# Performance work log

Measured on AMD Instinct MI355X. Metric: run time of the kernel, lower is better.

Reference implementation:

```python
import jax, jax.numpy as jnp
import numpy as np
from jax import lax

# Orthonormal 2x2 Haar (db1). Analysis uses dwt_scale per coefficient; the
# synthesis uses 0.5*idwt_scale so that dwt_scale=0.5, idwt_scale=1.0 gives a
# perfect round trip (Hadamard matrix M, M@M = 4I, M symmetric).
DWT_SCALE = 0.5
IDWT_SCALE = 1.0
WT_LEVELS = 3
STRIDE = 1
PAD = 1  # (kernel_size - 1) // 2


def dwt2(x, s):
    # x: (B, C, H, W) -> (B, C, 4, H/2, W/2), subband order LL, LH, HL, HH
    a = x[..., 0::2, 0::2]
    b = x[..., 0::2, 1::2]
    c = x[..., 1::2, 0::2]
    d = x[..., 1::2, 1::2]
    ll = (a + b + c + d) * s
    lh = (a - b + c - d) * s
    hl = (a + b - c - d) * s
    hh = (a - b - c + d) * s
    return jnp.stack([ll, lh, hl, hh], axis=2)


def idwt2(sub, s):
    # sub: (B, C, 4, h, w) -> (B, C, 2h, 2w); inverse of dwt2 when s = 0.5/ (4*dwt_s) * ... here Hadamard symmetric
    ll, lh, hl, hh = sub[:, :, 0], sub[:, :, 1], sub[:, :, 2], sub[:, :, 3]
    a = (ll + lh + hl + hh) * s
    b = (ll - lh + hl - hh) * s
    c = (ll + lh - hl - hh) * s
    d = (ll - lh - hl + hh) * s
    B, C, h, w = a.shape
    row0 = jnp.stack([a, b], axis=-1).reshape(B, C, h, 2 * w)
    row1 = jnp.stack([c, d], axis=-1).reshape(B, C, h, 2 * w)
    return jnp.stack([row0, row1], axis=-2).reshape(B, C, 2 * h, 2 * w)


def conv2d(x, w, stride, pad):
    return lax.conv_general_dilated(
        x, w, window_strides=(stride, stride),
        padding=[(pad, pad), (pad, pad)],
        dimension_numbers=('NCHW', 'OIHW', 'NCHW'))


def wtconv_core(x, weight):
    cout4 = weight.shape[0]
    cout = cout4 // 4
    curr_ll = x
    ll_levels, high_levels = [], []
    for _ in range(WT_LEVELS):
        sub = dwt2(curr_ll, DWT_SCALE)             # (B, C, 4, h, w)
        B, C, _, h, w = sub.shape
        y = conv2d(sub.reshape(B, C * 4, h, w), weight, STRIDE, PAD)
        y = y.reshape(B, cout, 4, h, w)
        ll_levels.append(y[:, :, 0])
        high_levels.append(y[:, :, 1:])
        curr_ll = sub[:, :, 0]                     # pre-conv LL feeds next level
    next_ll = jnp.zeros_like(ll_levels[-1])
    for ll, hi in zip(reversed(ll_levels), reversed(high_levels)):
        ll = ll + next_ll
        sub = jnp.concatenate([ll[:, :, None], hi], axis=2)
        next_ll = idwt2(sub, 0.5 * IDWT_SCALE)
    return next_ll


def setup_inputs() -> dict:
    key = jax.random.key(0)
    k1, k2, k3 = jax.random.split(key, 3)
    B, C, H, W = 8, 32, 224, 224
    K = 3
    x = jax.random.normal(k1, (B, C, H, W), dtype=jnp.float32)
    fan_in = C * 4 * K * K
    bound = np.sqrt(6.0 / ((1.0 + 2.236 ** 2) * fan_in))
    weight = jax.random.uniform(k2, (C * 4, C * 4, K, K), dtype=jnp.float32,
                                minval=-bound, maxval=bound)
    bias = jax.random.normal(k3, (C,), dtype=jnp.float32) * 0.01
    return {"x": x, "weight": weight, "bias": bias}


def reference(x, weight, bias):
    H, W = x.shape[-2:]
    pad_factor = 2 ** WT_LEVELS
    pad_h = (pad_factor - H % pad_factor) % pad_factor
    pad_w = (pad_factor - W % pad_factor) % pad_factor
    xp = x
    if pad_h > 0 or pad_w > 0:
        xp = jnp.pad(x, ((0, 0), (0, 0), (0, pad_h), (0, pad_w)), mode='reflect')
    out = wtconv_core(xp, weight)
    out = out[..., :H, :W]
    return out + bias[None, :, None, None]
```

## Files before the change

kernel.cpp:

```cpp
#include <hip/hip_runtime.h>

typedef __bf16 bf16_t;
typedef __bf16 bf16x4_t __attribute__((ext_vector_type(4)));
typedef __bf16 bf16x8_t __attribute__((ext_vector_type(8)));
typedef float f32x16_t __attribute__((ext_vector_type(16)));

#define AS_G(p) ((const __attribute__((address_space(1))) void*)(p))
#define AS_L(p) ((__attribute__((address_space(3))) void*)(p))
#define DRAIN_VM() asm volatile("s_waitcnt vmcnt(0)" ::: "memory")

__device__ __forceinline__ void repack_body(const float* __restrict__ w,
                                            bf16_t* __restrict__ wt2,
                                            int o) {
  int e = o & 7;
  int lane = (o >> 3) & 63;
  int f = o >> 9;
  int wc = f & 1;
  int nt = (f >> 1) & 1;
  int kc = (f >> 2) & 3;
  int hk = (f >> 4) & 1;
  int t = f >> 5;
  int oc = wc * 64 + nt * 32 + (lane & 31);
  int ic = (hk * 8 + kc * 2 + (lane >> 5)) * 8 + e;
  wt2[o] = (bf16_t)w[((size_t)oc * 128 + ic) * 9 + t];
}

__device__ __forceinline__ void dwt_body(const float* __restrict__ in,
                                         bf16_t* __restrict__ sub,
                                         float* __restrict__ llout,
                                         int h, int w, int bi, int i, int j0,
                                         bf16_t* lds) {
  const int tid = threadIdx.x;
  const int j = tid & 63;
  const int cg = tid >> 6;
  const int jg = j0 + j;
  const bool jok = jg < w;
  const int H2 = h * 2, W2 = w * 2;
  for (int c = cg; c < 32; c += 4) {
    float va = 0.f, vb = 0.f, vc = 0.f, vd = 0.f;
    if (jok) {
      const float2* p0 = (const float2*)(in + ((size_t)(bi * 32 + c) * H2 + 2 * i) * W2);
      const float2* p1 = (const float2*)(in + ((size_t)(bi * 32 + c) * H2 + 2 * i + 1) * W2);
      float2 r0 = p0[jg];
      float2 r1 = p1[jg];
      va = r0.x; vb = r0.y; vc = r1.x; vd = r1.y;
    }
    float ll = (va + vb + vc + vd) * 0.5f;
    float lh = (va - vb + vc - vd) * 0.5f;
    float hl = (va + vb - vc - vd) * 0.5f;
    float hh = (va - vb - vc + vd) * 0.5f;
    bf16x4_t q;
    q.x = (bf16_t)ll; q.y = (bf16_t)lh; q.z = (bf16_t)hl; q.w = (bf16_t)hh;
    *(bf16x4_t*)(&lds[j * 132 + c * 4]) = q;
    if (llout != nullptr && jok)
      llout[((size_t)(bi * 32 + c) * h + i) * w + jg] = ll;
  }
  __syncthreads();
  const size_t obase = ((size_t)bi * h + i) * w;
  for (int it = 0; it < 8; ++it) {
    int flat = it * 256 + tid;
    int jj = flat >> 5;
    int c4 = flat & 31;
    if (j0 + jj < w) {
      bf16x4_t q = *(const bf16x4_t*)(&lds[jj * 132 + c4 * 4]);
      *(bf16x4_t*)(sub + ((obase + j0 + jj) << 7) + c4 * 4) = q;
    }
  }
}

__global__ __launch_bounds__(256) void ll0r_kernel(const float* __restrict__ in,
                                                   float* __restrict__ llout,
                                                   const float* __restrict__ wsrc,
                                                   bf16_t* __restrict__ wt2,
                                                   int h, int w) {
  if (blockIdx.z == 8) {
    int bid = blockIdx.y * 2 + blockIdx.x;
    for (int o = bid * 256 + threadIdx.x; o < 147456; o += 224 * 256)
      repack_body(wsrc, wt2, o);
    return;
  }
  const int bi = blockIdx.z;
  const int i = blockIdx.y;
  const int jg = blockIdx.x * 64 + (threadIdx.x & 63);
  const int cg = threadIdx.x >> 6;
  if (jg >= w) return;
  const int H2 = h * 2, W2 = w * 2;
  for (int c = cg; c < 32; c += 4) {
    const float2* p0 = (const float2*)(in + ((size_t)(bi * 32 + c) * H2 + 2 * i) * W2);
    const float2* p1 = (const float2*)(in + ((size_t)(bi * 32 + c) * H2 + 2 * i + 1) * W2);
    float2 r0 = p0[jg];
    float2 r1 = p1[jg];
    llout[((size_t)(bi * 32 + c) * h + i) * w + jg] =
        (r0.x + r0.y + r1.x + r1.y) * 0.5f;
  }
}

__global__ __launch_bounds__(256) void dwt_kernel(const float* __restrict__ in,
                                                  bf16_t* __restrict__ sub,
                                                  float* __restrict__ llout,
                                                  int h, int w) {
  __shared__ __align__(16) bf16_t lds[64 * 132];
  dwt_body(in, sub, llout, h, w, blockIdx.z, blockIdx.y, blockIdx.x * 64, lds);
}

__device__ __forceinline__ void conv_idwt_tile(
    const bf16_t* __restrict__ sub, const bf16_t* __restrict__ wt2,
    const float* __restrict__ nll, const float* __restrict__ nllup,
    const float* __restrict__ bias, float* __restrict__ out,
    int h, int w, int bi, int y0, int x0, int och, uint4* smemV) {
  char* haloS = (char*)smemV;
  char* Bbuf = (char*)smemV + 23040;
  float* scr = (float*)((char*)smemV + 23040);
  const int tid = threadIdx.x;
  const size_t img_base = (size_t)bi * h * w;

  const int lane = tid & 63;
  const int wv = tid >> 6;
  const int m = lane & 31;
  const int hw_ = lane >> 5;
  const int il = wv * 2 + (m >> 4);
  const int jl = m & 15;
  const int pixA = il * 18 + jl;

  f32x16_t acc[2] = {};

  for (int hk = 0; hk < 2; ++hk) {
    if (hk) __syncthreads();
    for (int it = 0; it < 6; ++it) {
      int flat = it * 256 + tid;
      int pix = flat >> 3;
      int ch = flat & 7;
      if (pix < 180) {
        int r = pix / 18;
        int c = pix - r * 18;
        int gy = y0 + r - 1;
        int gx = x0 + c - 1;
        uint4 v = make_uint4(0u, 0u, 0u, 0u);
        if ((unsigned)gy < (unsigned)h && (unsigned)gx < (unsigned)w)
          v = *(const uint4*)(sub + ((img_base + (size_t)gy * w + gx) << 7) +
                              ((hk * 8 + ch) << 3));
        *(uint4*)(haloS + (pix << 7) + ((ch ^ (pix & 7)) << 4)) = v;
      }
    }
    {
      const int th0 = hk;
#pragma unroll
      for (int q = 0; q < 2; ++q) {
        const bf16_t* srcp = wt2 + (((th0 << 4) + (wv << 2) + (q << 1) + och) << 9) + (lane << 3);
        __builtin_amdgcn_global_load_lds(AS_G(srcp),
            AS_L(Bbuf + (((wv << 1) + q) << 10)), 16, 0, 0);
      }
    }
    DRAIN_VM();
    __syncthreads();

    int cur = 0;
    for (int t = 0; t < 9; ++t) {
      if (t < 8) {
        const int thn = ((t + 1) << 1) + hk;
#pragma unroll
        for (int q = 0; q < 2; ++q) {
          const bf16_t* srcp = wt2 + (((thn << 4) + (wv << 2) + (q << 1) + och) << 9) + (lane << 3);
          __builtin_amdgcn_global_load_lds(AS_G(srcp),
              AS_L(Bbuf + ((cur ^ 1) << 13) + (((wv << 1) + q) << 10)), 16, 0, 0);
        }
      }
      const int ky = t / 3;
      const int kx = t - ky * 3;
      const int pix0 = pixA + ky * 18 + kx;
      const int s0 = pix0 & 7;
      const char* hp0 = haloS + (pix0 << 7);
      const char* bp = Bbuf + (cur << 13) + (lane << 4);
#pragma unroll
      for (int kc = 0; kc < 4; ++kc) {
        bf16x8_t b0 = *(const bf16x8_t*)(bp + ((kc << 1) << 10));
        bf16x8_t b1 = *(const bf16x8_t*)(bp + (((kc << 1) + 1) << 10));
        const int cidx = kc * 2 + hw_;
        bf16x8_t a0 = *(const bf16x8_t*)(hp0 + ((cidx ^ s0) << 4));
        acc[0] = __builtin_amdgcn_mfma_f32_32x32x16_bf16(a0, b0, acc[0], 0, 0, 0);
        acc[1] = __builtin_amdgcn_mfma_f32_32x32x16_bf16(a0, b1, acc[1], 0, 0, 0);
      }
      DRAIN_VM();
      __syncthreads();
      cur ^= 1;
    }
  }

  const int W2 = w * 2;
  const int H2 = h * 2;
  const int hu = h >> 1, wu = w >> 1;
  const int mh_t = m >> 4;
  const int mm = m & 15;
  const int kw = mm >> 2;
  const int sw = mm & 3;

#pragma unroll
  for (int ph = 0; ph < 4; ++ph) {
    const int nt = ph >> 1;
    const int mh = ph & 1;
    if (ph) __syncthreads();
    if (mh_t == mh) {
#pragma unroll
      for (int reg = 0; reg < 16; ++reg) {
        int row = (reg & 3) + ((reg >> 2) << 3) + (hw_ << 2);
        int px = wv * 32 + row;
        scr[px * 17 + (kw << 2) + sw] = acc[nt][reg];
      }
    }
    __syncthreads();
#pragma unroll
    for (int it = 0; it < 2; ++it) {
      int idx = it * 256 + tid;
      int ox4 = idx & 7;
      int dy = (idx >> 3) & 1;
      int row = (idx >> 4) & 7;
      int k = (idx >> 7) & 3;
      int gy = y0 + row;
      int gx = x0 + ox4 * 2;
      if (gy >= h || gx >= w) continue;
      int p0 = row * 16 + ox4 * 2;
      int p1 = p0 + 1;
      float4 sa = *(const float4*)(&scr[p0 * 17 + (k << 2)]);
      float4 sb = *(const float4*)(&scr[p1 * 17 + (k << 2)]);
      float sg = dy ? -1.f : 1.f;
      float e0 = sa.x + sa.y + sg * (sa.z + sa.w);
      float e1 = sa.x - sa.y + sg * (sa.z - sa.w);
      float e2 = sb.x + sb.y + sg * (sb.z + sb.w);
      float e3 = sb.x - sb.y + sg * (sb.z - sb.w);
      int ch = och * 16 + nt * 8 + mh * 4 + k;
      float n0 = 0.f, n1 = 0.f;
      if (nll != nullptr) {
        const float* np = nll + ((size_t)(bi * 32 + ch) * h + gy) * w + gx;
        float2 nv = *(const float2*)np;
        n0 = nv.x; n1 = nv.y;
      }
      if (nllup != nullptr) {
        float u = nllup[((size_t)(bi * 32 + ch) * hu + (gy >> 1)) * wu + (gx >> 1)];
        n0 += 0.5f * u;
        n1 += 0.5f * u;
      }
      float bv = (bias != nullptr) ? bias[ch] : 0.f;
      float4 o;
      o.x = 0.5f * e0 + 0.5f * n0 + bv;
      o.y = 0.5f * e1 + 0.5f * n0 + bv;
      o.z = 0.5f * e2 + 0.5f * n1 + bv;
      o.w = 0.5f * e3 + 0.5f * n1 + bv;
      float* op = out + ((size_t)(bi * 32 + ch) * H2 + 2 * gy + dy) * W2 + 2 * gx;
      *(float4*)op = o;
    }
  }
}

__global__ __launch_bounds__(256, 4) void conv_idwt_kernel(
    const bf16_t* __restrict__ sub, const bf16_t* __restrict__ wt2,
    const float* __restrict__ nll, const float* __restrict__ nllup,
    const float* __restrict__ bias, float* __restrict__ out, int h, int w) {
  __shared__ uint4 smemV[2464];
  conv_idwt_tile(sub, wt2, nll, nllup, bias, out, h, w,
                 blockIdx.z, blockIdx.y * 8, (blockIdx.x >> 1) * 16,
                 blockIdx.x & 1, smemV);
}

__global__ __launch_bounds__(256, 4) void conv12s_kernel(
    const float* __restrict__ x, bf16_t* __restrict__ sub0,
    const bf16_t* __restrict__ sub1, const bf16_t* __restrict__ sub2,
    const bf16_t* __restrict__ wt2, float* __restrict__ nll1raw,
    float* __restrict__ nll2) {
  __shared__ uint4 smemV[2464];
  const int B = blockIdx.x;
  if (B >= 576) {
    int r = B - 576;
    int bx = r & 1;
    int rr = r >> 1;
    int i = rr % 112;
    int bi = rr / 112;
    dwt_body(x, sub0, nullptr, 112, 112, bi, i, bx * 64, (bf16_t*)smemV);
    return;
  }
  const bf16_t* sub;
  float* outp;
  int hh, bi, by, bx, och;
  if (B < 448) {
    och = B & 1;
    int q = B >> 1;
    bx = q & 3;
    int r = q >> 2;
    by = r % 7;
    bi = r / 7;
    sub = sub1; outp = nll1raw; hh = 56;
  } else {
    int lb = B - 448;
    och = lb & 1;
    int q = lb >> 1;
    bx = q & 1;
    int r = q >> 1;
    by = r & 3;
    bi = r >> 2;
    sub = sub2; outp = nll2; hh = 28;
  }
  conv_idwt_tile(sub, wt2, nullptr, nullptr, nullptr, outp, hh, hh,
                 bi, by * 8, bx * 16, och, smemV);
}

extern "C" void kernel_launch(void* const* d_in, const int* in_sizes, int n_in,
                              void* d_out, int out_size, void* d_ws, size_t ws_size,
                              hipStream_t stream) {
  if (ws_size < 66125824u) return;

  const float* x = (const float*)d_in[0];
  const float* weight = (const float*)d_in[1];
  const float* bias = (const float*)d_in[2];
  float* out = (float*)d_out;
  char* ws = (char*)d_ws;

  bf16_t* wt2 = (bf16_t*)(ws);
  bf16_t* sub0 = (bf16_t*)(ws + 294912);
  bf16_t* sub1 = (bf16_t*)(ws + 25985024);
  bf16_t* sub2 = (bf16_t*)(ws + 32407552);
  float* ll0 = (float*)(ws + 34013184);
  float* ll1 = (float*)(ws + 46858240);
  float* nll2 = (float*)(ws + 50069504);
  float* nll1 = (float*)(ws + 53280768);

  ll0r_kernel<<<dim3(2, 112, 9), 256, 0, stream>>>(x, ll0, weight, wt2, 112, 112);
  dwt_kernel<<<dim3(1, 56, 8), 256, 0, stream>>>(ll0, sub1, ll1, 56, 56);
  dwt_kernel<<<dim3(1, 28, 8), 256, 0, stream>>>(ll1, sub2, nullptr, 28, 28);
  conv12s_kernel<<<2368, 256, 0, stream>>>(x, sub0, sub1, sub2, wt2, nll1, nll2);
  conv_idwt_kernel<<<dim3(14, 14, 8), 256, 0, stream>>>(sub0, wt2, nll1, nll2, bias, out, 112, 112);
}
```

Measured before the change: 181.4 us.

## Replace level-0 conv with larger 16x16 tile, all-output-channel 512-thread kernel

Adds a dedicated level-0 conv+IDWT kernel that processes a 16x16 pixel tile with all 32 output channels per block using 8 waves, each wave computing a 2x2 grid of MFMA tiles. This reuses each loaded halo across all output channels and more pixel rows, reducing redundant global halo loads and the halo-overhead ratio compared with the previous 8x16, half-channel tiles. The shared tile function loses its residual/bias epilogue since it now only serves the lower levels. The cost is larger LDS use per block, 512-thread blocks, fewer blocks (392), and more epilogue phases with extra barriers, which may lower occupancy.

```diff
diff --git a/kernel.cpp b/kernel.cpp
--- a/kernel.cpp
+++ b/kernel.cpp
@@ -188,7 +188,6 @@
 
   const int W2 = w * 2;
   const int H2 = h * 2;
-  const int hu = h >> 1, wu = w >> 1;
   const int mh_t = m >> 4;
   const int mm = m & 15;
   const int kw = mm >> 2;
@@ -228,37 +227,12 @@
       float e2 = sb.x + sb.y + sg * (sb.z + sb.w);
       float e3 = sb.x - sb.y + sg * (sb.z - sb.w);
       int ch = och * 16 + nt * 8 + mh * 4 + k;
-      float n0 = 0.f, n1 = 0.f;
-      if (nll != nullptr) {
-        const float* np = nll + ((size_t)(bi * 32 + ch) * h + gy) * w + gx;
-        float2 nv = *(const float2*)np;
-        n0 = nv.x; n1 = nv.y;
-      }
-      if (nllup != nullptr) {
-        float u = nllup[((size_t)(bi * 32 + ch) * hu + (gy >> 1)) * wu + (gx >> 1)];
-        n0 += 0.5f * u;
-        n1 += 0.5f * u;
-      }
-      float bv = (bias != nullptr) ? bias[ch] : 0.f;
+      float* op = out + ((size_t)(bi * 32 + ch) * H2 + 2 * gy + dy) * W2 + 2 * gx;
       float4 o;
-      o.x = 0.5f * e0 + 0.5f * n0 + bv;
-      o.y = 0.5f * e1 + 0.5f * n0 + bv;
-      o.z = 0.5f * e2 + 0.5f * n1 + bv;
-      o.w = 0.5f * e3 + 0.5f * n1 + bv;
-      float* op = out + ((size_t)(bi * 32 + ch) * H2 + 2 * gy + dy) * W2 + 2 * gx;
+      o.x = 0.5f * e0; o.y = 0.5f * e1; o.z = 0.5f * e2; o.w = 0.5f * e3;
       *(float4*)op = o;
     }
   }
-}
-
-__global__ __launch_bounds__(256, 4) void conv_idwt_kernel(
-    const bf16_t* __restrict__ sub, const bf16_t* __restrict__ wt2,
-    const float* __restrict__ nll, const float* __restrict__ nllup,
-    const float* __restrict__ bias, float* __restrict__ out, int h, int w) {
-  __shared__ uint4 smemV[2464];
-  conv_idwt_tile(sub, wt2, nll, nllup, bias, out, h, w,
-                 blockIdx.z, blockIdx.y * 8, (blockIdx.x >> 1) * 16,
-                 blockIdx.x & 1, smemV);
 }
 
 __global__ __launch_bounds__(256, 4) void conv12s_kernel(
@@ -302,6 +276,170 @@
                  bi, by * 8, bx * 16, och, smemV);
 }
 
+__global__ __launch_bounds__(512, 4) void conv0_kernel(
+    const bf16_t* __restrict__ sub, const bf16_t* __restrict__ wt2,
+    const float* __restrict__ nll, const float* __restrict__ nllup,
+    const float* __restrict__ bias, float* __restrict__ out, int h, int w) {
+  __shared__ uint4 smemV[4640];
+  char* haloS = (char*)smemV;
+  char* Bbuf = (char*)smemV + 41472;
+  float* scr = (float*)((char*)smemV + 41472);
+
+  const int tid = threadIdx.x;
+  const int bi = blockIdx.z;
+  const int y0 = blockIdx.y * 16;
+  const int x0 = blockIdx.x * 16;
+  const size_t img_base = (size_t)bi * h * w;
+
+  const int lane = tid & 63;
+  const int wv = tid >> 6;
+  const int wm = wv >> 1;
+  const int wo = wv & 1;
+  const int m = lane & 31;
+  const int hw_ = lane >> 5;
+  const int pixA = (wm * 4 + (m >> 4)) * 18 + (m & 15);
+
+  f32x16_t acc[2][2] = {};
+
+  for (int hk = 0; hk < 2; ++hk) {
+    if (hk) __syncthreads();
+    for (int it = 0; it < 6; ++it) {
+      int flat = it * 512 + tid;
+      int pix = flat >> 3;
+      int ch = flat & 7;
+      if (pix < 324) {
+        int r = pix / 18;
+        int c = pix - r * 18;
+        int gy = y0 + r - 1;
+        int gx = x0 + c - 1;
+        uint4 v = make_uint4(0u, 0u, 0u, 0u);
+        if ((unsigned)gy < (unsigned)h && (unsigned)gx < (unsigned)w)
+          v = *(const uint4*)(sub + ((img_base + (size_t)gy * w + gx) << 7) +
+                              ((hk * 8 + ch) << 3));
+        *(uint4*)(haloS + (pix << 7) + ((ch ^ (pix & 7)) << 4)) = v;
+      }
+    }
+    {
+      const int th0 = hk;
+#pragma unroll
+      for (int q = 0; q < 2; ++q) {
+        const int fi = wv * 2 + q;
+        const bf16_t* srcp = wt2 + (((th0 << 4) + fi) << 9) + (lane << 3);
+        __builtin_amdgcn_global_load_lds(AS_G(srcp),
+            AS_L(Bbuf + (fi << 10)), 16, 0, 0);
+      }
+    }
+    DRAIN_VM();
+    __syncthreads();
+
+    int cur = 0;
+    for (int t = 0; t < 9; ++t) {
+      if (t < 8) {
+        const int thn = ((t + 1) << 1) + hk;
+#pragma unroll
+        for (int q = 0; q < 2; ++q) {
+          const int fi = wv * 2 + q;
+          const bf16_t* srcp = wt2 + (((thn << 4) + fi) << 9) + (lane << 3);
+          __builtin_amdgcn_global_load_lds(AS_G(srcp),
+              AS_L(Bbuf + ((cur ^ 1) << 14) + (fi << 10)), 16, 0, 0);
+        }
+      }
+      const int ky = t / 3;
+      const int kx = t - ky * 3;
+      const int pix0 = pixA + ky * 18 + kx;
+      const int pix1 = pix0 + 36;
+      const int s0 = pix0 & 7;
+      const int s1 = pix1 & 7;
+      const char* hp0 = haloS + (pix0 << 7);
+      const char* hp1 = haloS + (pix1 << 7);
+      const char* bp = Bbuf + (cur << 14) + (lane << 4);
+#pragma unroll
+      for (int kc = 0; kc < 4; ++kc) {
+        bf16x8_t b0 = *(const bf16x8_t*)(bp + (((kc << 2) + wo) << 10));
+        bf16x8_t b1 = *(const bf16x8_t*)(bp + (((kc << 2) + 2 + wo) << 10));
+        const int cidx = kc * 2 + hw_;
+        bf16x8_t a0 = *(const bf16x8_t*)(hp0 + ((cidx ^ s0) << 4));
+        bf16x8_t a1 = *(const bf16x8_t*)(hp1 + ((cidx ^ s1) << 4));
+        acc[0][0] = __builtin_amdgcn_mfma_f32_32x32x16_bf16(a0, b0, acc[0][0], 0, 0, 0);
+        acc[0][1] = __builtin_amdgcn_mfma_f32_32x32x16_bf16(a0, b1, acc[0][1], 0, 0, 0);
+        acc[1][0] = __builtin_amdgcn_mfma_f32_32x32x16_bf16(a1, b0, acc[1][0], 0, 0, 0);
+        acc[1][1] = __builtin_amdgcn_mfma_f32_32x32x16_bf16(a1, b1, acc[1][1], 0, 0, 0);
+      }
+      DRAIN_VM();
+      __syncthreads();
+      cur ^= 1;
+    }
+  }
+
+  const int W2 = w * 2;
+  const int H2 = h * 2;
+  const int hu = h >> 1, wu = w >> 1;
+  const int mh_t = m >> 4;
+  const int mm = m & 15;
+  const int kw = mm >> 2;
+  const int sw = mm & 3;
+
+#pragma unroll
+  for (int ph = 0; ph < 8; ++ph) {
+    const int wo_p = ph >> 2;
+    const int nt_p = (ph >> 1) & 1;
+    const int mh_p = ph & 1;
+    if (ph) __syncthreads();
+    if (wo == wo_p && mh_t == mh_p) {
+#pragma unroll
+      for (int mt = 0; mt < 2; ++mt) {
+#pragma unroll
+        for (int reg = 0; reg < 16; ++reg) {
+          int rowi = (reg & 3) + ((reg >> 2) << 3) + (hw_ << 2);
+          int px = (wm * 4 + mt * 2 + (rowi >> 4)) * 16 + (rowi & 15);
+          scr[px * 17 + (kw << 2) + sw] = acc[mt][nt_p][reg];
+        }
+      }
+    }
+    __syncthreads();
+#pragma unroll
+    for (int it = 0; it < 2; ++it) {
+      int idx = it * 512 + tid;
+      int ox4 = idx & 7;
+      int dy = (idx >> 3) & 1;
+      int row = (idx >> 4) & 15;
+      int k = (idx >> 8) & 3;
+      int gy = y0 + row;
+      int gx = x0 + ox4 * 2;
+      if (gy >= h || gx >= w) continue;
+      int p0 = row * 16 + ox4 * 2;
+      int p1 = p0 + 1;
+      float4 sa = *(const float4*)(&scr[p0 * 17 + (k << 2)]);
+      float4 sb = *(const float4*)(&scr[p1 * 17 + (k << 2)]);
+      float sg = dy ? -1.f : 1.f;
+      float e0 = sa.x + sa.y + sg * (sa.z + sa.w);
+      float e1 = sa.x - sa.y + sg * (sa.z - sa.w);
+      float e2 = sb.x + sb.y + sg * (sb.z + sb.w);
+      float e3 = sb.x - sb.y + sg * (sb.z - sb.w);
+      int ch = wo_p * 16 + nt_p * 8 + mh_p * 4 + k;
+      float n0 = 0.f, n1 = 0.f;
+      if (nll != nullptr) {
+        const float* np = nll + ((size_t)(bi * 32 + ch) * h + gy) * w + gx;
+        float2 nv = *(const float2*)np;
+        n0 = nv.x; n1 = nv.y;
+      }
+      if (nllup != nullptr) {
+        float u = nllup[((size_t)(bi * 32 + ch) * hu + (gy >> 1)) * wu + (gx >> 1)];
+        n0 += 0.5f * u;
+        n1 += 0.5f * u;
+      }
+      float bv = (bias != nullptr) ? bias[ch] : 0.f;
+      float4 o;
+      o.x = 0.5f * e0 + 0.5f * n0 + bv;
+      o.y = 0.5f * e1 + 0.5f * n0 + bv;
+      o.z = 0.5f * e2 + 0.5f * n1 + bv;
+      o.w = 0.5f * e3 + 0.5f * n1 + bv;
+      float* op = out + ((size_t)(bi * 32 + ch) * H2 + 2 * gy + dy) * W2 + 2 * gx;
+      *(float4*)op = o;
+    }
+  }
+}
+
 extern "C" void kernel_launch(void* const* d_in, const int* in_sizes, int n_in,
                               void* d_out, int out_size, void* d_ws, size_t ws_size,
                               hipStream_t stream) {
@@ -326,5 +464,5 @@
   dwt_kernel<<<dim3(1, 56, 8), 256, 0, stream>>>(ll0, sub1, ll1, 56, 56);
   dwt_kernel<<<dim3(1, 28, 8), 256, 0, stream>>>(ll1, sub2, nullptr, 28, 28);
   conv12s_kernel<<<2368, 256, 0, stream>>>(x, sub0, sub1, sub2, wt2, nll1, nll2);
-  conv_idwt_kernel<<<dim3(14, 14, 8), 256, 0, stream>>>(sub0, wt2, nll1, nll2, bias, out, 112, 112);
-}
+  conv0_kernel<<<dim3(7, 7, 8), 512, 0, stream>>>(sub0, wt2, nll1, nll2, bias, out, 112, 112);
+}
```

New measurement: 204.4 us. 12.7% more time.
